# Kernel optimization log

Measured on AMD Instinct MI355X. Metric: run time of the kernel, lower is better.

Reference implementation:

```python
import jax, jax.numpy as jnp
import numpy as np

GROUPS = 32
HEADS = 4
EPS_GN = 1e-5
EPS_DEN = 1e-6


def group_norm(x, gamma, beta):
    b, c, h, w = x.shape
    xg = x.reshape(b, GROUPS, (c // GROUPS) * h * w)
    mu = xg.mean(axis=-1, keepdims=True)
    var = xg.var(axis=-1, keepdims=True)
    xn = ((xg - mu) * jax.lax.rsqrt(var + EPS_GN)).reshape(b, c, h, w)
    return xn * gamma[None, :, None, None] + beta[None, :, None, None]


def setup_inputs() -> dict:
    key = jax.random.key(0)
    ks = jax.random.split(key, 4)
    b, c, h, w = 16, 256, 64, 64
    x = jax.random.normal(ks[0], (b, c, h, w), dtype=jnp.float32)
    gamma = jnp.ones((c,), jnp.float32)
    beta = jnp.zeros((c,), jnp.float32)
    w_qkv = jax.random.normal(ks[1], (3 * c, c), jnp.float32) * (1.0 / np.sqrt(c))
    b_qkv = jnp.zeros((3 * c,), jnp.float32)
    w_out = jax.random.normal(ks[2], (c, c), jnp.float32) * (1.0 / np.sqrt(c))
    b_out = jnp.zeros((c,), jnp.float32)
    return {"x": x, "gamma": gamma, "beta": beta, "w_qkv": w_qkv,
            "b_qkv": b_qkv, "w_out": w_out, "b_out": b_out}


def reference(x, gamma, beta, w_qkv, b_qkv, w_out, b_out):
    b, c, h, w = x.shape
    d = c // HEADS
    n = h * w
    xn = group_norm(x, gamma, beta)
    # 1x1 conv == channel GEMM: [b,3c,h,w]
    qkv = jnp.einsum('bchw,oc->bohw', xn, w_qkv) + b_qkv[None, :, None, None]
    q, k, v = jnp.split(qkv, 3, axis=1)
    # b (heads d) h w -> b heads d n
    q = q.reshape(b, HEADS, d, n)
    k = k.reshape(b, HEADS, d, n)
    v = v.reshape(b, HEADS, d, n)
    q = jax.nn.elu(q) + 1.0
    k = jax.nn.elu(k) + 1.0
    k_sum = k.sum(axis=-1)                                 # [b,H,d]
    kv = jnp.einsum('bhdn,bhen->bhde', k, v)               # [b,H,d,d]
    out = jnp.einsum('bhde,bhdn->bhen', kv, q)             # [b,H,d,n]
    denom = jnp.einsum('bhdn,bhd->bhn', q, k_sum)          # [b,H,n]
    out = out / (denom[:, :, None, :] + EPS_DEN)
    out = out.reshape(b, c, h, w)
    out = jnp.einsum('bchw,oc->bohw', out, w_out) + b_out[None, :, None, None]
    return out + x
```

## Files before the change

kernel.cpp:

```cpp
#include <hip/hip_runtime.h>
#include <stdint.h>

#define BATCH 16
#define CH    256
#define NSP   4096
#define NH    4
#define HD    64

typedef __attribute__((ext_vector_type(8))) short bf16x8;
typedef __attribute__((ext_vector_type(4))) float f32x4;
typedef __attribute__((ext_vector_type(4))) unsigned int u32x4;

__device__ __forceinline__ short f2bf(float f) {
    union { float f; unsigned u; } v; v.f = f;
    unsigned r = (v.u + 0x7fffu + ((v.u >> 16) & 1u)) >> 16;
    return (short)r;
}
__device__ __forceinline__ float bf2f(short s) {
    union { float f; unsigned u; } v; v.u = ((unsigned)(unsigned short)s) << 16;
    return v.f;
}

__global__ __launch_bounds__(256) void k_pre(
        const float* __restrict__ x, const float* __restrict__ wq, const float* __restrict__ wo,
        float* __restrict__ mu, float* __restrict__ rstd,
        short* __restrict__ wq_bf, short* __restrict__ wo_bf) {
    int bg = blockIdx.x;
    if (bg < 512) {
        const float4* p = (const float4*)(x + (size_t)bg * 32768);
        float s = 0.f, sq = 0.f;
        for (int i = threadIdx.x; i < 8192; i += 256) {
            float4 v = p[i];
            s  += v.x + v.y + v.z + v.w;
            sq += v.x * v.x + v.y * v.y + v.z * v.z + v.w * v.w;
        }
        for (int off = 32; off; off >>= 1) { s += __shfl_down(s, off); sq += __shfl_down(sq, off); }
        __shared__ float ls[4], lq[4];
        int w = threadIdx.x >> 6;
        if ((threadIdx.x & 63) == 0) { ls[w] = s; lq[w] = sq; }
        __syncthreads();
        if (threadIdx.x == 0) {
            float S = ls[0] + ls[1] + ls[2] + ls[3];
            float Q = lq[0] + lq[1] + lq[2] + lq[3];
            float m = S / 32768.f;
            float var = Q / 32768.f - m * m;
            mu[bg] = m; rstd[bg] = rsqrtf(var + 1e-5f);
        }
    } else {
        int idx = ((bg - 512) * 256 + threadIdx.x) * 4;
        float4 v;
        short* dst;
        if (idx < 196608) { v = *(const float4*)(wq + idx); dst = wq_bf + idx; }
        else              { v = *(const float4*)(wo + (idx - 196608)); dst = wo_bf + (idx - 196608); }
        unsigned p0 = ((unsigned)(unsigned short)f2bf(v.x)) | (((unsigned)(unsigned short)f2bf(v.y)) << 16);
        unsigned p1 = ((unsigned)(unsigned short)f2bf(v.z)) | (((unsigned)(unsigned short)f2bf(v.w)) << 16);
        uint2 pk; pk.x = p0; pk.y = p1;
        *(uint2*)dst = pk;
    }
}

__global__ __launch_bounds__(256) void k_gnqkv(
        const float* __restrict__ x, const float* __restrict__ gamma, const float* __restrict__ beta,
        const float* __restrict__ mu, const float* __restrict__ rstd,
        const short* __restrict__ wq_bf, const float* __restrict__ b_qkv,
        short* __restrict__ q_t, short* __restrict__ kvp_bf, float* __restrict__ ksp) {
    int b = blockIdx.y;
    __shared__ short Blds[64 * 264];
    __shared__ union UR {
        struct { short kst[64 * 72]; short vst[64 * 72]; } s;
        short cst[64 * 136];
    } R;
    int t = threadIdx.x, lane = t & 63, wv = t >> 6, lr = lane & 15, quad = lane >> 4;

    for (int it = 0; it < 2; it++) {
        int nt = blockIdx.x * 2 + it;
        int n0 = nt * 64;

        {
            const float* xb = x + (size_t)b * CH * NSP;
            int m = t & 15, cq = t >> 4;
            #pragma unroll 4
            for (int cb = 0; cb < 16; cb++) {
                int c = cb * 16 + cq;
                int g = c >> 3;
                float sc = rstd[b * 32 + g] * gamma[c];
                float sh = beta[c] - mu[b * 32 + g] * sc;
                float4 v = *(const float4*)(xb + (size_t)c * NSP + n0 + m * 4);
                float vv[4] = {v.x, v.y, v.z, v.w};
                #pragma unroll
                for (int j = 0; j < 4; j++) {
                    int n = m * 4 + j;
                    int cc = c ^ (((n >> 4) & 3) << 3);
                    Blds[n * 264 + cc] = f2bf(vv[j] * sc + sh);
                }
            }
        }
        __syncthreads();

        for (int h = 0; h < 4; h++) {
            int br0 = (wv < 2 ? 256 : 512) + h * 64;
            int sub = (wv & 1) * 32;
            const short* wr = wq_bf + (size_t)(br0 + sub + lr) * 256 + quad * 8;
            bf16x8 A0[8], A1[8];
            #pragma unroll
            for (int kk = 0; kk < 8; kk++) {
                A0[kk] = *(const bf16x8*)(wr + kk * 32);
                A1[kk] = *(const bf16x8*)(wr + 16 * 256 + kk * 32);
            }
            f32x4 acc[2][4] = {};
            #pragma unroll
            for (int kk = 0; kk < 8; kk++) {
                bf16x8 bfr[4];
                #pragma unroll
                for (int ni = 0; ni < 4; ni++) {
                    int rr = ni * 16 + lr;
                    bfr[ni] = *(const bf16x8*)(Blds + rr * 264 + ((kk * 32 + quad * 8) ^ (((rr >> 4) & 3) << 3)));
                }
                #pragma unroll
                for (int ni = 0; ni < 4; ni++) {
                    acc[0][ni] = __builtin_amdgcn_mfma_f32_16x16x32_bf16(A0[kk], bfr[ni], acc[0][ni], 0, 0, 0);
                    acc[1][ni] = __builtin_amdgcn_mfma_f32_16x16x32_bf16(A1[kk], bfr[ni], acc[1][ni], 0, 0, 0);
                }
            }
            __syncthreads();
            short* dst = (wv < 2) ? R.s.kst : R.s.vst;
            bool is_k = (wv < 2);
            #pragma unroll
            for (int mi = 0; mi < 2; mi++)
              #pragma unroll
              for (int ni = 0; ni < 4; ni++)
                #pragma unroll
                for (int r = 0; r < 4; r++) {
                    int ol = sub + mi * 16 + quad * 4 + r;
                    int nl = ni * 16 + lr;
                    float v = acc[mi][ni][r] + b_qkv[br0 + ol];
                    if (is_k) v = v > 0.f ? v + 1.f : __expf(v);
                    dst[ol * 72 + nl] = f2bf(v);
                }
            __syncthreads();
            {
                int d = t >> 2, nq = (t & 3) * 16;
                float s = 0.f;
                #pragma unroll
                for (int j = 0; j < 16; j++) s += bf2f(R.s.kst[d * 72 + nq + j]);
                s += __shfl_down(s, 2);
                s += __shfl_down(s, 1);
                if ((t & 3) == 0) ksp[((size_t)(b * 4 + h) * 64 + nt) * 64 + d] = s;
            }
            f32x4 acc2[4] = {};
            #pragma unroll
            for (int kk = 0; kk < 64; kk += 32) {
                bf16x8 af = *(const bf16x8*)(R.s.vst + (wv * 16 + lr) * 72 + kk + quad * 8);
                bf16x8 bfk[4];
                #pragma unroll
                for (int ni = 0; ni < 4; ni++)
                    bfk[ni] = *(const bf16x8*)(R.s.kst + (ni * 16 + lr) * 72 + kk + quad * 8);
                #pragma unroll
                for (int ni = 0; ni < 4; ni++)
                    acc2[ni] = __builtin_amdgcn_mfma_f32_16x16x32_bf16(af, bfk[ni], acc2[ni], 0, 0, 0);
            }
            short* kvdst = kvp_bf + ((size_t)(b * 4 + h) * 64 + nt) * 4096;
            #pragma unroll
            for (int ni = 0; ni < 4; ni++)
                #pragma unroll
                for (int r = 0; r < 4; r++)
                    kvdst[(wv * 16 + quad * 4 + r) * 64 + ni * 16 + lr] = f2bf(acc2[ni][r]);
        }

        for (int mtq = 0; mtq < 2; mtq++) {
            int wm = wv * 32;
            const short* wr = wq_bf + (size_t)(mtq * 128 + wm + lr) * 256 + quad * 8;
            bf16x8 A0[8], A1[8];
            #pragma unroll
            for (int kk = 0; kk < 8; kk++) {
                A0[kk] = *(const bf16x8*)(wr + kk * 32);
                A1[kk] = *(const bf16x8*)(wr + 16 * 256 + kk * 32);
            }
            f32x4 acc[2][4] = {};
            #pragma unroll
            for (int kk = 0; kk < 8; kk++) {
                bf16x8 bfr[4];
                #pragma unroll
                for (int ni = 0; ni < 4; ni++) {
                    int rr = ni * 16 + lr;
                    bfr[ni] = *(const bf16x8*)(Blds + rr * 264 + ((kk * 32 + quad * 8) ^ (((rr >> 4) & 3) << 3)));
                }
                #pragma unroll
                for (int ni = 0; ni < 4; ni++) {
                    acc[0][ni] = __builtin_amdgcn_mfma_f32_16x16x32_bf16(A0[kk], bfr[ni], acc[0][ni], 0, 0, 0);
                    acc[1][ni] = __builtin_amdgcn_mfma_f32_16x16x32_bf16(A1[kk], bfr[ni], acc[1][ni], 0, 0, 0);
                }
            }
            __syncthreads();
            #pragma unroll
            for (int mi = 0; mi < 2; mi++)
              #pragma unroll
              for (int ni = 0; ni < 4; ni++)
                #pragma unroll
                for (int r = 0; r < 4; r++) {
                    int ol = wm + mi * 16 + quad * 4 + r;
                    int nl = ni * 16 + lr;
                    float v = acc[mi][ni][r] + b_qkv[mtq * 128 + ol];
                    v = v > 0.f ? v + 1.f : __expf(v);
                    R.cst[nl * 136 + ol] = f2bf(v);
                }
            __syncthreads();
            #pragma unroll
            for (int i = 0; i < 4; i++) {
                int ch = t + i * 256;
                int row = ch >> 4, o8 = (ch & 15) * 8;
                int hh = mtq * 2 + (o8 >> 6), d0 = o8 & 63;
                *(u32x4*)(q_t + ((size_t)(b * 4 + hh) * NSP + n0 + row) * HD + d0) =
                    *(const u32x4*)(R.cst + row * 136 + o8);
            }
        }
    }
}

__global__ __launch_bounds__(256) void k_kv_reduce(
        const short* __restrict__ kvp_bf, const float* __restrict__ ksp,
        short* __restrict__ kvT_bf, float* __restrict__ ksum_g) {
    int p = blockIdx.x, bh = blockIdx.y;
    int t = threadIdx.x, lane = t & 63, grp = t >> 6;
    int chunk = p * 64 + lane;
    const short* base = kvp_bf + (size_t)bh * 64 * 4096 + chunk * 8;
    float s[8] = {};
    for (int ntc = grp * 16; ntc < grp * 16 + 16; ntc++) {
        bf16x8 v = *(const bf16x8*)(base + (size_t)ntc * 4096);
        #pragma unroll
        for (int j = 0; j < 8; j++) s[j] += bf2f(v[j]);
    }
    __shared__ float red[4][64][8];
    if (grp) {
        #pragma unroll
        for (int j = 0; j < 8; j++) red[grp][lane][j] = s[j];
    }
    __syncthreads();
    if (grp == 0) {
        bf16x8 rv;
        #pragma unroll
        for (int j = 0; j < 8; j++) {
            float v = s[j] + red[1][lane][j] + red[2][lane][j] + red[3][lane][j];
            rv[j] = f2bf(v);
        }
        *(bf16x8*)(kvT_bf + (size_t)bh * 4096 + chunk * 8) = rv;
    }
    if (p == 0) {
        const float* kb = ksp + (size_t)bh * 64 * 64 + lane;
        float ss = 0.f;
        for (int ntc = grp * 16; ntc < grp * 16 + 16; ntc++) ss += kb[(size_t)ntc * 64];
        __syncthreads();
        red[grp][lane][0] = ss;
        __syncthreads();
        if (grp == 0) ksum_g[bh * 64 + lane] = ss + red[1][lane][0] + red[2][lane][0] + red[3][lane][0];
    }
}

__global__ __launch_bounds__(256) void k_attn_out(
        const short* __restrict__ q_t, const short* __restrict__ kvT_bf,
        const float* __restrict__ ksum_g, const short* __restrict__ wo_bf,
        const float* __restrict__ b_out, const float* __restrict__ x,
        float* __restrict__ out) {
    int b = blockIdx.y;
    __shared__ short Battn[64 * 264];
    __shared__ float dnl[4][64];
    int t = threadIdx.x, lane = t & 63, wv = t >> 6, lr = lane & 15, quad = lane >> 4;

    for (int it = 0; it < 2; it++) {
        int nt = blockIdx.x * 2 + it;
        int n0 = nt * 64;

        {
            const short* qp = q_t + ((size_t)(b * 4 + wv) * NSP + n0 + lane) * HD;
            const float* ks = ksum_g + (b * 4 + wv) * 64;
            float s = 0.f;
            #pragma unroll
            for (int c8 = 0; c8 < 8; c8++) {
                bf16x8 qv = *(const bf16x8*)(qp + c8 * 8);
                #pragma unroll
                for (int j = 0; j < 8; j++) s += bf2f(qv[j]) * ks[c8 * 8 + j];
            }
            dnl[wv][lane] = 1.f / (s + 1e-6f);
        }
        __syncthreads();

        for (int h = 0; h < 4; h++) {
            size_t bh = (size_t)(b * 4 + h);
            const short* qbase = q_t + (bh * NSP + n0) * HD;
            const short* kvbase = kvT_bf + bh * 4096;
            bf16x8 af[2], bfr[2][4];
            #pragma unroll
            for (int kz = 0; kz < 2; kz++) {
                af[kz] = *(const bf16x8*)(qbase + (wv * 16 + lr) * HD + kz * 32 + quad * 8);
                #pragma unroll
                for (int ni = 0; ni < 4; ni++)
                    bfr[kz][ni] = *(const bf16x8*)(kvbase + (ni * 16 + lr) * HD + kz * 32 + quad * 8);
            }
            f32x4 acc[4] = {};
            #pragma unroll
            for (int kz = 0; kz < 2; kz++)
                #pragma unroll
                for (int ni = 0; ni < 4; ni++)
                    acc[ni] = __builtin_amdgcn_mfma_f32_16x16x32_bf16(af[kz], bfr[kz][ni], acc[ni], 0, 0, 0);
            #pragma unroll
            for (int ni = 0; ni < 4; ni++)
                #pragma unroll
                for (int r = 0; r < 4; r++) {
                    int n = wv * 16 + quad * 4 + r;
                    Battn[n * 264 + h * 64 + ni * 16 + lr] = f2bf(acc[ni][r] * dnl[h][n]);
                }
        }
        __syncthreads();

        for (int p = 0; p < 2; p++) {
            int rbase = p * 128 + wv * 32;
            const short* wr = wo_bf + (size_t)(rbase + lr) * 256 + quad * 8;
            bf16x8 A0[8], A1[8];
            #pragma unroll
            for (int kk = 0; kk < 8; kk++) {
                A0[kk] = *(const bf16x8*)(wr + kk * 32);
                A1[kk] = *(const bf16x8*)(wr + 16 * 256 + kk * 32);
            }
            f32x4 acc[2][4] = {};
            #pragma unroll
            for (int kk = 0; kk < 8; kk++) {
                bf16x8 bfr[4];
                #pragma unroll
                for (int ni = 0; ni < 4; ni++)
                    bfr[ni] = *(const bf16x8*)(Battn + (ni * 16 + lr) * 264 + kk * 32 + quad * 8);
                #pragma unroll
                for (int ni = 0; ni < 4; ni++) {
                    acc[0][ni] = __builtin_amdgcn_mfma_f32_16x16x32_bf16(A0[kk], bfr[ni], acc[0][ni], 0, 0, 0);
                    acc[1][ni] = __builtin_amdgcn_mfma_f32_16x16x32_bf16(A1[kk], bfr[ni], acc[1][ni], 0, 0, 0);
                }
            }
            #pragma unroll
            for (int mi = 0; mi < 2; mi++)
              #pragma unroll
              for (int ni = 0; ni < 4; ni++)
                #pragma unroll
                for (int r = 0; r < 4; r++) {
                    int o = rbase + mi * 16 + quad * 4 + r;
                    int nl = ni * 16 + lr;
                    size_t idx = ((size_t)b * CH + o) * NSP + n0 + nl;
                    out[idx] = acc[mi][ni][r] + b_out[o] + x[idx];
                }
        }
    }
}

extern "C" void kernel_launch(void* const* d_in, const int* in_sizes, int n_in,
                              void* d_out, int out_size, void* d_ws, size_t ws_size,
                              hipStream_t stream) {
    const float* x     = (const float*)d_in[0];
    const float* gamma = (const float*)d_in[1];
    const float* beta  = (const float*)d_in[2];
    const float* w_qkv = (const float*)d_in[3];
    const float* b_qkv = (const float*)d_in[4];
    const float* w_out = (const float*)d_in[5];
    const float* b_out = (const float*)d_in[6];
    float* out = (float*)d_out;

    char* ws = (char*)d_ws;
    size_t off = 0;
    float* mu     = (float*)(ws + off); off += 2048;
    float* rstd   = (float*)(ws + off); off += 2048;
    short* wq_bf  = (short*)(ws + off); off += (size_t)768 * 256 * 2;
    short* wo_bf  = (short*)(ws + off); off += (size_t)256 * 256 * 2;
    short* q_t    = (short*)(ws + off); off += (size_t)BATCH * NSP * CH * 2;
    short* kvp_bf = (short*)(ws + off); off += (size_t)64 * 64 * 4096 * 2;
    float* ksp    = (float*)(ws + off); off += (size_t)64 * 64 * 64 * 4;
    short* kvT_bf = (short*)(ws + off); off += (size_t)64 * 4096 * 2;
    float* ksum_g = (float*)(ws + off); off += (size_t)64 * 64 * 4;

    if (ws_size < off) return;

    k_pre<<<768, 256, 0, stream>>>(x, w_qkv, w_out, mu, rstd, wq_bf, wo_bf);
    k_gnqkv<<<dim3(32, 16), 256, 0, stream>>>(x, gamma, beta, mu, rstd, wq_bf, b_qkv, q_t, kvp_bf, ksp);
    k_kv_reduce<<<dim3(8, 64), 256, 0, stream>>>(kvp_bf, ksp, kvT_bf, ksum_g);
    k_attn_out<<<dim3(32, 16), 256, 0, stream>>>(q_t, kvT_bf, ksum_g, wo_bf, b_out, x, out);
}
```

Measured before the change: 307.9 us.

## Use one tile per block and stage q/kv tiles in LDS for attention

```diff
diff --git a/kernel.cpp b/kernel.cpp
--- a/kernel.cpp
+++ b/kernel.cpp
@@ -64,7 +64,8 @@
         const float* __restrict__ mu, const float* __restrict__ rstd,
         const short* __restrict__ wq_bf, const float* __restrict__ b_qkv,
         short* __restrict__ q_t, short* __restrict__ kvp_bf, float* __restrict__ ksp) {
-    int b = blockIdx.y;
+    int b = blockIdx.y, nt = blockIdx.x;
+    int n0 = nt * 64;
     __shared__ short Blds[64 * 264];
     __shared__ union UR {
         struct { short kst[64 * 72]; short vst[64 * 72]; } s;
@@ -72,147 +73,142 @@
     } R;
     int t = threadIdx.x, lane = t & 63, wv = t >> 6, lr = lane & 15, quad = lane >> 4;
 
-    for (int it = 0; it < 2; it++) {
-        int nt = blockIdx.x * 2 + it;
-        int n0 = nt * 64;
-
+    {
+        const float* xb = x + (size_t)b * CH * NSP;
+        int m = t & 15, cq = t >> 4;
+        #pragma unroll 4
+        for (int cb = 0; cb < 16; cb++) {
+            int c = cb * 16 + cq;
+            int g = c >> 3;
+            float sc = rstd[b * 32 + g] * gamma[c];
+            float sh = beta[c] - mu[b * 32 + g] * sc;
+            float4 v = *(const float4*)(xb + (size_t)c * NSP + n0 + m * 4);
+            float vv[4] = {v.x, v.y, v.z, v.w};
+            #pragma unroll
+            for (int j = 0; j < 4; j++) {
+                int n = m * 4 + j;
+                int cc = c ^ (((n >> 4) & 3) << 3);
+                Blds[n * 264 + cc] = f2bf(vv[j] * sc + sh);
+            }
+        }
+    }
+    __syncthreads();
+
+    for (int h = 0; h < 4; h++) {
+        int br0 = (wv < 2 ? 256 : 512) + h * 64;
+        int sub = (wv & 1) * 32;
+        const short* wr = wq_bf + (size_t)(br0 + sub + lr) * 256 + quad * 8;
+        bf16x8 A0[8], A1[8];
+        #pragma unroll
+        for (int kk = 0; kk < 8; kk++) {
+            A0[kk] = *(const bf16x8*)(wr + kk * 32);
+            A1[kk] = *(const bf16x8*)(wr + 16 * 256 + kk * 32);
+        }
+        f32x4 acc[2][4] = {};
+        #pragma unroll
+        for (int kk = 0; kk < 8; kk++) {
+            bf16x8 bfr[4];
+            #pragma unroll
+            for (int ni = 0; ni < 4; ni++) {
+                int rr = ni * 16 + lr;
+                bfr[ni] = *(const bf16x8*)(Blds + rr * 264 + ((kk * 32 + quad * 8) ^ (((rr >> 4) & 3) << 3)));
+            }
+            #pragma unroll
+            for (int ni = 0; ni < 4; ni++) {
+                acc[0][ni] = __builtin_amdgcn_mfma_f32_16x16x32_bf16(A0[kk], bfr[ni], acc[0][ni], 0, 0, 0);
+                acc[1][ni] = __builtin_amdgcn_mfma_f32_16x16x32_bf16(A1[kk], bfr[ni], acc[1][ni], 0, 0, 0);
+            }
+        }
+        __syncthreads();
+        short* dst = (wv < 2) ? R.s.kst : R.s.vst;
+        bool is_k = (wv < 2);
+        #pragma unroll
+        for (int mi = 0; mi < 2; mi++)
+          #pragma unroll
+          for (int ni = 0; ni < 4; ni++)
+            #pragma unroll
+            for (int r = 0; r < 4; r++) {
+                int ol = sub + mi * 16 + quad * 4 + r;
+                int nl = ni * 16 + lr;
+                float v = acc[mi][ni][r] + b_qkv[br0 + ol];
+                if (is_k) v = v > 0.f ? v + 1.f : __expf(v);
+                dst[ol * 72 + nl] = f2bf(v);
+            }
+        __syncthreads();
         {
-            const float* xb = x + (size_t)b * CH * NSP;
-            int m = t & 15, cq = t >> 4;
-            #pragma unroll 4
-            for (int cb = 0; cb < 16; cb++) {
-                int c = cb * 16 + cq;
-                int g = c >> 3;
-                float sc = rstd[b * 32 + g] * gamma[c];
-                float sh = beta[c] - mu[b * 32 + g] * sc;
-                float4 v = *(const float4*)(xb + (size_t)c * NSP + n0 + m * 4);
-                float vv[4] = {v.x, v.y, v.z, v.w};
-                #pragma unroll
-                for (int j = 0; j < 4; j++) {
-                    int n = m * 4 + j;
-                    int cc = c ^ (((n >> 4) & 3) << 3);
-                    Blds[n * 264 + cc] = f2bf(vv[j] * sc + sh);
-                }
-            }
-        }
-        __syncthreads();
-
-        for (int h = 0; h < 4; h++) {
-            int br0 = (wv < 2 ? 256 : 512) + h * 64;
-            int sub = (wv & 1) * 32;
-            const short* wr = wq_bf + (size_t)(br0 + sub + lr) * 256 + quad * 8;
-            bf16x8 A0[8], A1[8];
-            #pragma unroll
-            for (int kk = 0; kk < 8; kk++) {
-                A0[kk] = *(const bf16x8*)(wr + kk * 32);
-                A1[kk] = *(const bf16x8*)(wr + 16 * 256 + kk * 32);
-            }
-            f32x4 acc[2][4] = {};
-            #pragma unroll
-            for (int kk = 0; kk < 8; kk++) {
-                bf16x8 bfr[4];
-                #pragma unroll
-                for (int ni = 0; ni < 4; ni++) {
-                    int rr = ni * 16 + lr;
-                    bfr[ni] = *(const bf16x8*)(Blds + rr * 264 + ((kk * 32 + quad * 8) ^ (((rr >> 4) & 3) << 3)));
-                }
-                #pragma unroll
-                for (int ni = 0; ni < 4; ni++) {
-                    acc[0][ni] = __builtin_amdgcn_mfma_f32_16x16x32_bf16(A0[kk], bfr[ni], acc[0][ni], 0, 0, 0);
-                    acc[1][ni] = __builtin_amdgcn_mfma_f32_16x16x32_bf16(A1[kk], bfr[ni], acc[1][ni], 0, 0, 0);
-                }
-            }
-            __syncthreads();
-            short* dst = (wv < 2) ? R.s.kst : R.s.vst;
-            bool is_k = (wv < 2);
-            #pragma unroll
-            for (int mi = 0; mi < 2; mi++)
-              #pragma unroll
-              for (int ni = 0; ni < 4; ni++)
-                #pragma unroll
-                for (int r = 0; r < 4; r++) {
-                    int ol = sub + mi * 16 + quad * 4 + r;
-                    int nl = ni * 16 + lr;
-                    float v = acc[mi][ni][r] + b_qkv[br0 + ol];
-                    if (is_k) v = v > 0.f ? v + 1.f : __expf(v);
-                    dst[ol * 72 + nl] = f2bf(v);
-                }
-            __syncthreads();
-            {
-                int d = t >> 2, nq = (t & 3) * 16;
-                float s = 0.f;
-                #pragma unroll
-                for (int j = 0; j < 16; j++) s += bf2f(R.s.kst[d * 72 + nq + j]);
-                s += __shfl_down(s, 2);
-                s += __shfl_down(s, 1);
-                if ((t & 3) == 0) ksp[((size_t)(b * 4 + h) * 64 + nt) * 64 + d] = s;
-            }
-            f32x4 acc2[4] = {};
-            #pragma unroll
-            for (int kk = 0; kk < 64; kk += 32) {
-                bf16x8 af = *(const bf16x8*)(R.s.vst + (wv * 16 + lr) * 72 + kk + quad * 8);
-                bf16x8 bfk[4];
-                #pragma unroll
-                for (int ni = 0; ni < 4; ni++)
-                    bfk[ni] = *(const bf16x8*)(R.s.kst + (ni * 16 + lr) * 72 + kk + quad * 8);
-                #pragma unroll
-                for (int ni = 0; ni < 4; ni++)
-                    acc2[ni] = __builtin_amdgcn_mfma_f32_16x16x32_bf16(af, bfk[ni], acc2[ni], 0, 0, 0);
-            }
-            short* kvdst = kvp_bf + ((size_t)(b * 4 + h) * 64 + nt) * 4096;
-            #pragma unroll
-            for (int ni = 0; ni < 4; ni++)
-                #pragma unroll
-                for (int r = 0; r < 4; r++)
-                    kvdst[(wv * 16 + quad * 4 + r) * 64 + ni * 16 + lr] = f2bf(acc2[ni][r]);
-        }
-
-        for (int mtq = 0; mtq < 2; mtq++) {
-            int wm = wv * 32;
-            const short* wr = wq_bf + (size_t)(mtq * 128 + wm + lr) * 256 + quad * 8;
-            bf16x8 A0[8], A1[8];
-            #pragma unroll
-            for (int kk = 0; kk < 8; kk++) {
-                A0[kk] = *(const bf16x8*)(wr + kk * 32);
-                A1[kk] = *(const bf16x8*)(wr + 16 * 256 + kk * 32);
-            }
-            f32x4 acc[2][4] = {};
-            #pragma unroll
-            for (int kk = 0; kk < 8; kk++) {
-                bf16x8 bfr[4];
-                #pragma unroll
-                for (int ni = 0; ni < 4; ni++) {
-                    int rr = ni * 16 + lr;
-                    bfr[ni] = *(const bf16x8*)(Blds + rr * 264 + ((kk * 32 + quad * 8) ^ (((rr >> 4) & 3) << 3)));
-                }
-                #pragma unroll
-                for (int ni = 0; ni < 4; ni++) {
-                    acc[0][ni] = __builtin_amdgcn_mfma_f32_16x16x32_bf16(A0[kk], bfr[ni], acc[0][ni], 0, 0, 0);
-                    acc[1][ni] = __builtin_amdgcn_mfma_f32_16x16x32_bf16(A1[kk], bfr[ni], acc[1][ni], 0, 0, 0);
-                }
-            }
-            __syncthreads();
-            #pragma unroll
-            for (int mi = 0; mi < 2; mi++)
-              #pragma unroll
-              for (int ni = 0; ni < 4; ni++)
-                #pragma unroll
-                for (int r = 0; r < 4; r++) {
-                    int ol = wm + mi * 16 + quad * 4 + r;
-                    int nl = ni * 16 + lr;
-                    float v = acc[mi][ni][r] + b_qkv[mtq * 128 + ol];
-                    v = v > 0.f ? v + 1.f : __expf(v);
-                    R.cst[nl * 136 + ol] = f2bf(v);
-                }
-            __syncthreads();
-            #pragma unroll
-            for (int i = 0; i < 4; i++) {
-                int ch = t + i * 256;
-                int row = ch >> 4, o8 = (ch & 15) * 8;
-                int hh = mtq * 2 + (o8 >> 6), d0 = o8 & 63;
-                *(u32x4*)(q_t + ((size_t)(b * 4 + hh) * NSP + n0 + row) * HD + d0) =
-                    *(const u32x4*)(R.cst + row * 136 + o8);
-            }
+            int d = t >> 2, nq = (t & 3) * 16;
+            float s = 0.f;
+            #pragma unroll
+            for (int j = 0; j < 16; j++) s += bf2f(R.s.kst[d * 72 + nq + j]);
+            s += __shfl_down(s, 2);
+            s += __shfl_down(s, 1);
+            if ((t & 3) == 0) ksp[((size_t)(b * 4 + h) * 64 + nt) * 64 + d] = s;
+        }
+        f32x4 acc2[4] = {};
+        #pragma unroll
+        for (int kk = 0; kk < 64; kk += 32) {
+            bf16x8 af = *(const bf16x8*)(R.s.vst + (wv * 16 + lr) * 72 + kk + quad * 8);
+            bf16x8 bfk[4];
+            #pragma unroll
+            for (int ni = 0; ni < 4; ni++)
+                bfk[ni] = *(const bf16x8*)(R.s.kst + (ni * 16 + lr) * 72 + kk + quad * 8);
+            #pragma unroll
+            for (int ni = 0; ni < 4; ni++)
+                acc2[ni] = __builtin_amdgcn_mfma_f32_16x16x32_bf16(af, bfk[ni], acc2[ni], 0, 0, 0);
+        }
+        short* kvdst = kvp_bf + ((size_t)(b * 4 + h) * 64 + nt) * 4096;
+        #pragma unroll
+        for (int ni = 0; ni < 4; ni++)
+            #pragma unroll
+            for (int r = 0; r < 4; r++)
+                kvdst[(wv * 16 + quad * 4 + r) * 64 + ni * 16 + lr] = f2bf(acc2[ni][r]);
+    }
+
+    for (int mtq = 0; mtq < 2; mtq++) {
+        int wm = wv * 32;
+        const short* wr = wq_bf + (size_t)(mtq * 128 + wm + lr) * 256 + quad * 8;
+        bf16x8 A0[8], A1[8];
+        #pragma unroll
+        for (int kk = 0; kk < 8; kk++) {
+            A0[kk] = *(const bf16x8*)(wr + kk * 32);
+            A1[kk] = *(const bf16x8*)(wr + 16 * 256 + kk * 32);
+        }
+        f32x4 acc[2][4] = {};
+        #pragma unroll
+        for (int kk = 0; kk < 8; kk++) {
+            bf16x8 bfr[4];
+            #pragma unroll
+            for (int ni = 0; ni < 4; ni++) {
+                int rr = ni * 16 + lr;
+                bfr[ni] = *(const bf16x8*)(Blds + rr * 264 + ((kk * 32 + quad * 8) ^ (((rr >> 4) & 3) << 3)));
+            }
+            #pragma unroll
+            for (int ni = 0; ni < 4; ni++) {
+                acc[0][ni] = __builtin_amdgcn_mfma_f32_16x16x32_bf16(A0[kk], bfr[ni], acc[0][ni], 0, 0, 0);
+                acc[1][ni] = __builtin_amdgcn_mfma_f32_16x16x32_bf16(A1[kk], bfr[ni], acc[1][ni], 0, 0, 0);
+            }
+        }
+        __syncthreads();
+        #pragma unroll
+        for (int mi = 0; mi < 2; mi++)
+          #pragma unroll
+          for (int ni = 0; ni < 4; ni++)
+            #pragma unroll
+            for (int r = 0; r < 4; r++) {
+                int ol = wm + mi * 16 + quad * 4 + r;
+                int nl = ni * 16 + lr;
+                float v = acc[mi][ni][r] + b_qkv[mtq * 128 + ol];
+                v = v > 0.f ? v + 1.f : __expf(v);
+                R.cst[nl * 136 + ol] = f2bf(v);
+            }
+        __syncthreads();
+        #pragma unroll
+        for (int i = 0; i < 4; i++) {
+            int ch = t + i * 256;
+            int row = ch >> 4, o8 = (ch & 15) * 8;
+            int hh = mtq * 2 + (o8 >> 6), d0 = o8 & 63;
+            *(u32x4*)(q_t + ((size_t)(b * 4 + hh) * NSP + n0 + row) * HD + d0) =
+                *(const u32x4*)(R.cst + row * 136 + o8);
         }
     }
 }
@@ -261,91 +257,100 @@
         const float* __restrict__ ksum_g, const short* __restrict__ wo_bf,
         const float* __restrict__ b_out, const float* __restrict__ x,
         float* __restrict__ out) {
-    int b = blockIdx.y;
+    int b = blockIdx.y, nt = blockIdx.x;
+    int n0 = nt * 64;
     __shared__ short Battn[64 * 264];
-    __shared__ float dnl[4][64];
+    __shared__ short ql[64 * 72];
+    __shared__ short kvl[64 * 72];
+    __shared__ float dnp[4][64];
     int t = threadIdx.x, lane = t & 63, wv = t >> 6, lr = lane & 15, quad = lane >> 4;
 
-    for (int it = 0; it < 2; it++) {
-        int nt = blockIdx.x * 2 + it;
-        int n0 = nt * 64;
-
+    for (int h = 0; h < 4; h++) {
+        int bh = b * 4 + h;
+        #pragma unroll
+        for (int i = 0; i < 2; i++) {
+            int ch = t + i * 256;
+            int row = ch >> 3, dc = (ch & 7) * 8;
+            *(u32x4*)(ql + row * 72 + dc) =
+                *(const u32x4*)(q_t + ((size_t)bh * NSP + n0 + row) * HD + dc);
+            *(u32x4*)(kvl + row * 72 + dc) =
+                *(const u32x4*)(kvT_bf + (size_t)bh * 4096 + row * 64 + dc);
+        }
+        __syncthreads();
         {
-            const short* qp = q_t + ((size_t)(b * 4 + wv) * NSP + n0 + lane) * HD;
-            const float* ks = ksum_g + (b * 4 + wv) * 64;
+            int n = t & 63, q0 = wv * 16;
+            const float* ks = ksum_g + bh * 64 + q0;
             float s = 0.f;
             #pragma unroll
-            for (int c8 = 0; c8 < 8; c8++) {
-                bf16x8 qv = *(const bf16x8*)(qp + c8 * 8);
+            for (int j = 0; j < 16; j += 8) {
+                bf16x8 qv = *(const bf16x8*)(ql + n * 72 + q0 + j);
                 #pragma unroll
-                for (int j = 0; j < 8; j++) s += bf2f(qv[j]) * ks[c8 * 8 + j];
-            }
-            dnl[wv][lane] = 1.f / (s + 1e-6f);
-        }
-        __syncthreads();
-
-        for (int h = 0; h < 4; h++) {
-            size_t bh = (size_t)(b * 4 + h);
-            const short* qbase = q_t + (bh * NSP + n0) * HD;
-            const short* kvbase = kvT_bf + bh * 4096;
-            bf16x8 af[2], bfr[2][4];
-            #pragma unroll
-            for (int kz = 0; kz < 2; kz++) {
-                af[kz] = *(const bf16x8*)(qbase + (wv * 16 + lr) * HD + kz * 32 + quad * 8);
-                #pragma unroll
-                for (int ni = 0; ni < 4; ni++)
-                    bfr[kz][ni] = *(const bf16x8*)(kvbase + (ni * 16 + lr) * HD + kz * 32 + quad * 8);
-            }
-            f32x4 acc[4] = {};
-            #pragma unroll
-            for (int kz = 0; kz < 2; kz++)
-                #pragma unroll
-                for (int ni = 0; ni < 4; ni++)
-                    acc[ni] = __builtin_amdgcn_mfma_f32_16x16x32_bf16(af[kz], bfr[kz][ni], acc[ni], 0, 0, 0);
-            #pragma unroll
-            for (int ni = 0; ni < 4; ni++)
-                #pragma unroll
-                for (int r = 0; r < 4; r++) {
-                    int n = wv * 16 + quad * 4 + r;
-                    Battn[n * 264 + h * 64 + ni * 16 + lr] = f2bf(acc[ni][r] * dnl[h][n]);
-                }
-        }
-        __syncthreads();
-
-        for (int p = 0; p < 2; p++) {
-            int rbase = p * 128 + wv * 32;
-            const short* wr = wo_bf + (size_t)(rbase + lr) * 256 + quad * 8;
-            bf16x8 A0[8], A1[8];
-            #pragma unroll
-            for (int kk = 0; kk < 8; kk++) {
-                A0[kk] = *(const bf16x8*)(wr + kk * 32);
-                A1[kk] = *(const bf16x8*)(wr + 16 * 256 + kk * 32);
-            }
-            f32x4 acc[2][4] = {};
-            #pragma unroll
-            for (int kk = 0; kk < 8; kk++) {
-                bf16x8 bfr[4];
-                #pragma unroll
-                for (int ni = 0; ni < 4; ni++)
-                    bfr[ni] = *(const bf16x8*)(Battn + (ni * 16 + lr) * 264 + kk * 32 + quad * 8);
-                #pragma unroll
-                for (int ni = 0; ni < 4; ni++) {
-                    acc[0][ni] = __builtin_amdgcn_mfma_f32_16x16x32_bf16(A0[kk], bfr[ni], acc[0][ni], 0, 0, 0);
-                    acc[1][ni] = __builtin_amdgcn_mfma_f32_16x16x32_bf16(A1[kk], bfr[ni], acc[1][ni], 0, 0, 0);
-                }
-            }
-            #pragma unroll
-            for (int mi = 0; mi < 2; mi++)
-              #pragma unroll
-              for (int ni = 0; ni < 4; ni++)
-                #pragma unroll
-                for (int r = 0; r < 4; r++) {
-                    int o = rbase + mi * 16 + quad * 4 + r;
-                    int nl = ni * 16 + lr;
-                    size_t idx = ((size_t)b * CH + o) * NSP + n0 + nl;
-                    out[idx] = acc[mi][ni][r] + b_out[o] + x[idx];
-                }
-        }
+                for (int u = 0; u < 8; u++) s += bf2f(qv[u]) * ks[j + u];
+            }
+            dnp[wv][n] = s;
+        }
+        f32x4 acc[4] = {};
+        #pragma unroll
+        for (int kk = 0; kk < 64; kk += 32) {
+            bf16x8 af = *(const bf16x8*)(ql + (wv * 16 + lr) * 72 + kk + quad * 8);
+            bf16x8 bfr[4];
+            #pragma unroll
+            for (int ni = 0; ni < 4; ni++)
+                bfr[ni] = *(const bf16x8*)(kvl + (ni * 16 + lr) * 72 + kk + quad * 8);
+            #pragma unroll
+            for (int ni = 0; ni < 4; ni++)
+                acc[ni] = __builtin_amdgcn_mfma_f32_16x16x32_bf16(af, bfr[ni], acc[ni], 0, 0, 0);
+        }
+        __syncthreads();
+        float dn[4];
+        #pragma unroll
+        for (int r = 0; r < 4; r++) {
+            int n = wv * 16 + quad * 4 + r;
+            dn[r] = 1.f / (dnp[0][n] + dnp[1][n] + dnp[2][n] + dnp[3][n] + 1e-6f);
+        }
+        #pragma unroll
+        for (int ni = 0; ni < 4; ni++)
+            #pragma unroll
+            for (int r = 0; r < 4; r++) {
+                int n = wv * 16 + quad * 4 + r;
+                Battn[n * 264 + h * 64 + ni * 16 + lr] = f2bf(acc[ni][r] * dn[r]);
+            }
+        __syncthreads();
+    }
+
+    for (int p = 0; p < 2; p++) {
+        int rbase = p * 128 + wv * 32;
+        const short* wr = wo_bf + (size_t)(rbase + lr) * 256 + quad * 8;
+        bf16x8 A0[8], A1[8];
+        #pragma unroll
+        for (int kk = 0; kk < 8; kk++) {
+            A0[kk] = *(const bf16x8*)(wr + kk * 32);
+            A1[kk] = *(const bf16x8*)(wr + 16 * 256 + kk * 32);
+        }
+        f32x4 acc[2][4] = {};
+        #pragma unroll
+        for (int kk = 0; kk < 8; kk++) {
+            bf16x8 bfr[4];
+            #pragma unroll
+            for (int ni = 0; ni < 4; ni++)
+                bfr[ni] = *(const bf16x8*)(Battn + (ni * 16 + lr) * 264 + kk * 32 + quad * 8);
+            #pragma unroll
+            for (int ni = 0; ni < 4; ni++) {
+                acc[0][ni] = __builtin_amdgcn_mfma_f32_16x16x32_bf16(A0[kk], bfr[ni], acc[0][ni], 0, 0, 0);
+                acc[1][ni] = __builtin_amdgcn_mfma_f32_16x16x32_bf16(A1[kk], bfr[ni], acc[1][ni], 0, 0, 0);
+            }
+        }
+        #pragma unroll
+        for (int mi = 0; mi < 2; mi++)
+          #pragma unroll
+          for (int ni = 0; ni < 4; ni++)
+            #pragma unroll
+            for (int r = 0; r < 4; r++) {
+                int o = rbase + mi * 16 + quad * 4 + r;
+                int nl = ni * 16 + lr;
+                size_t idx = ((size_t)b * CH + o) * NSP + n0 + nl;
+                out[idx] = acc[mi][ni][r] + b_out[o] + x[idx];
+            }
     }
 }
 
@@ -376,7 +381,7 @@
     if (ws_size < off) return;
 
     k_pre<<<768, 256, 0, stream>>>(x, w_qkv, w_out, mu, rstd, wq_bf, wo_bf);
-    k_gnqkv<<<dim3(32, 16), 256, 0, stream>>>(x, gamma, beta, mu, rstd, wq_bf, b_qkv, q_t, kvp_bf, ksp);
+    k_gnqkv<<<dim3(64, 16), 256, 0, stream>>>(x, gamma, beta, mu, rstd, wq_bf, b_qkv, q_t, kvp_bf, ksp);
     k_kv_reduce<<<dim3(8, 64), 256, 0, stream>>>(kvp_bf, ksp, kvT_bf, ksum_g);
-    k_attn_out<<<dim3(32, 16), 256, 0, stream>>>(q_t, kvT_bf, ksum_g, wo_bf, b_out, x, out);
-}
+    k_attn_out<<<dim3(64, 16), 256, 0, stream>>>(q_t, kvT_bf, ksum_g, wo_bf, b_out, x, out);
+}
```

Result: faster. 278.5 us (-9.6%).
